# Kernel tuning notes

Hardware: AMD Instinct MI355X
Metric: run time of the kernel (lower is better)

## Reference

```python
import jax, jax.numpy as jnp
import numpy as np

B, M, P, L, L_EVAL = 16, 32, 16, 1024, 2048


def setup_inputs() -> dict:
    key = jax.random.key(0)
    ks = jax.random.split(key, 6)
    # sorted event times per (B, P) path via cumsum of positive steps
    steps = jax.random.uniform(ks[0], (B, P, L), minval=0.01, maxval=0.1)
    event_times = jnp.cumsum(steps, axis=-1)  # [B, P, L], strictly increasing
    norm_constants = jax.random.uniform(ks[1], (B,), minval=0.5, maxval=1.5)
    # queries on the ORIGINAL (unnormalised) time axis, spanning the event range
    t_max = event_times[..., -1]  # [B, P]
    q_norm = jax.random.uniform(ks[2], (B, P, L_EVAL)) * (1.05 * t_max)[..., None]
    query_times = q_norm * norm_constants[:, None, None]
    mu = jax.random.uniform(ks[3], (B, M, P, L), minval=0.05, maxval=1.0)
    alpha = jax.random.uniform(ks[4], (B, M, P, L), minval=0.05, maxval=2.0)
    beta = jax.random.uniform(ks[5], (B, M, P, L), minval=0.1, maxval=3.0)
    return {
        "query_times": query_times,
        "event_times": event_times,
        "mu": mu,
        "alpha": alpha,
        "beta": beta,
        "norm_constants": norm_constants,
    }


def _batched_searchsorted(a, v):
    # a: [B, P, L] sorted along last dim, v: [B, P, Q] -> int32 [B, P, Q]
    f = lambda av, vv: jnp.searchsorted(av, vv, side="left")
    return jax.vmap(jax.vmap(f))(a, v)


def reference(query_times, event_times, mu, alpha, beta, norm_constants):
    Bq, Pq, Le = query_times.shape
    Mm = mu.shape[1]
    # normalized_times=False path: map queries onto the normalised axis
    q_norm = query_times / norm_constants[:, None, None]  # [B, P, Le]
    # index of the latest event strictly before each query time
    last_idx = _batched_searchsorted(event_times, q_norm) - 1  # [B, P, Le]
    idx = jnp.clip(last_idx, 0, None)
    gidx = jnp.broadcast_to(idx[:, None, :, :], (Bq, Mm, Pq, Le))
    mu_last = jnp.take_along_axis(mu, gidx, axis=3)
    alpha_last = jnp.take_along_axis(alpha, gidx, axis=3)
    beta_last = jnp.take_along_axis(beta, gidx, axis=3)
    t_last = jnp.take_along_axis(event_times, idx, axis=2)  # [B, P, Le]
    t_last = jnp.where(last_idx == -1, jnp.zeros_like(t_last), t_last)
    delta_t = (q_norm - t_last)[:, None, :, :]  # [B, 1, P, Le]
    intensity = mu_last + (alpha_last - mu_last) * jnp.exp(-beta_last * delta_t)
    # map intensity back to the original scale
    intensity = intensity / norm_constants[:, None, None, None]
    return intensity
```

## Files before the change

kernel.cpp:

```cpp
#include <hip/hip_runtime.h>


constexpr int B  = 16;
constexpr int M  = 32;
constexpr int P  = 16;
constexpr int L  = 1024;
constexpr int LE = 2048;

__global__ __launch_bounds__(1024)
void hawkes_kernel(const float* __restrict__ qt,
                   const float* __restrict__ ev,
                   const float* __restrict__ mu,
                   const float* __restrict__ al,
                   const float* __restrict__ be,
                   const float* __restrict__ nc,
                   float* __restrict__ out)
{
    __shared__ float  s_ev[L];
    __shared__ float4 s_prm[2][L];

    const int bp = blockIdx.x;
    const int b  = bp >> 4;
    const int p  = bp & (P - 1);
    const int t  = threadIdx.x;

    const float norm     = nc[b];
    const float inv_norm = (float)(1.0 / (double)norm);

    const size_t row0 = ((size_t)b * M * P + p) * L;
    const size_t mstr = (size_t)P * L;

    const float e_in = ev[(size_t)bp * L + t];
    float rA_mu = mu[row0 + t],        rA_al = al[row0 + t],        rA_be = be[row0 + t];
    float rB_mu = mu[row0 + mstr + t], rB_al = al[row0 + mstr + t], rB_be = be[row0 + mstr + t];

    s_ev[t]     = e_in;
    s_prm[0][t] = make_float4(rA_mu, rA_al, rA_be, 0.0f);

    __syncthreads();

    const float2 q2 = *reinterpret_cast<const float2*>(qt + (size_t)bp * LE + 2 * t);
    int   idx0, idx1;
    float dt0, dt1;
    {
        float qn[2] = { __fmul_rn(q2.x, inv_norm), __fmul_rn(q2.y, inv_norm) };
        int lo[2] = {0, 0}, hi[2] = {L, L};
#pragma unroll
        for (int s = 0; s < 11; ++s) {
#pragma unroll
            for (int k = 0; k < 2; ++k) {
                if (lo[k] < hi[k]) {
                    const int mid = (lo[k] + hi[k]) >> 1;
                    if (s_ev[mid] < qn[k]) lo[k] = mid + 1; else hi[k] = mid;
                }
            }
        }
        const int l0 = lo[0] - 1, l1 = lo[1] - 1;
        idx0 = (l0 < 0) ? 0 : l0;   dt0 = qn[0] - ((l0 < 0) ? 0.0f : s_ev[idx0]);
        idx1 = (l1 < 0) ? 0 : l1;   dt1 = qn[1] - ((l1 < 0) ? 0.0f : s_ev[idx1]);
    }

    float* const obase = out + ((size_t)b * M * P + p) * LE + 2 * t;
    const size_t ostr  = (size_t)P * LE;

#define COMPUTE_ROW(BUF, mrow)                                                  \
    {                                                                           \
        const float4 v0 = s_prm[BUF][idx0];                                     \
        const float4 v1 = s_prm[BUF][idx1];                                     \
        float2 o;                                                               \
        o.x = fmaf(v0.y - v0.x, __expf(-v0.z * dt0), v0.x) * inv_norm;          \
        o.y = fmaf(v1.y - v1.x, __expf(-v1.z * dt1), v1.x) * inv_norm;          \
        *reinterpret_cast<float2*>(obase + (size_t)(mrow) * ostr) = o;          \
    }

#pragma unroll 1
    for (int m = 0; m < M; m += 2) {
        if (m + 2 < M) {
            const size_t r = row0 + (size_t)(m + 2) * mstr;
            rA_mu = mu[r + t];  rA_al = al[r + t];  rA_be = be[r + t];
        }
        COMPUTE_ROW(0, m)
        s_prm[1][t] = make_float4(rB_mu, rB_al, rB_be, 0.0f);
        __syncthreads();

        if (m + 3 < M) {
            const size_t r = row0 + (size_t)(m + 3) * mstr;
            rB_mu = mu[r + t];  rB_al = al[r + t];  rB_be = be[r + t];
        }
        COMPUTE_ROW(1, m + 1)
        if (m + 2 < M) {
            s_prm[0][t] = make_float4(rA_mu, rA_al, rA_be, 0.0f);
        }
        __syncthreads();
    }
#undef COMPUTE_ROW
}

extern "C" void kernel_launch(void* const* d_in, const int* in_sizes, int n_in,
                              void* d_out, int out_size, void* d_ws, size_t ws_size,
                              hipStream_t stream) {
    const float* qt = (const float*)d_in[0];
    const float* ev = (const float*)d_in[1];
    const float* mu = (const float*)d_in[2];
    const float* al = (const float*)d_in[3];
    const float* be = (const float*)d_in[4];
    const float* nc = (const float*)d_in[5];
    float* out = (float*)d_out;

    hawkes_kernel<<<B * P, 1024, 0, stream>>>(qt, ev, mu, al, be, nc, out);
}
```

Baseline: 33.83 us.

## Stage parameters as packed bf16 in shared memory, 16 rows per sync phase

Replaces the two-row double-buffered float4 staging with two phases of 16 rows each. All 16 rows' mu/alpha/beta are loaded up front into registers, packed as bf16 into uint2 shared slots, then gathered. This cuts the number of barriers and puts more loads in flight per thread. The bf16 packing halves shared-memory footprint and gather width but rounds the parameters to 8-bit mantissa, which risks exceeding the accuracy tolerance. It also greatly raises register pressure at 1024 threads per block.

New measurement: 35.11 us. 3.8% more time.

```diff
diff --git a/kernel.cpp b/kernel.cpp
--- a/kernel.cpp
+++ b/kernel.cpp
@@ -6,6 +6,12 @@
 constexpr int P  = 16;
 constexpr int L  = 1024;
 constexpr int LE = 2048;
+constexpr int RC = 16;
+
+__device__ __forceinline__ unsigned bf16rne(float x) {
+    const unsigned u = __float_as_uint(x);
+    return (u + 0x7FFFu + ((u >> 16) & 1u)) >> 16;
+}
 
 __global__ __launch_bounds__(1024)
 void hawkes_kernel(const float* __restrict__ qt,
@@ -16,8 +22,8 @@
                    const float* __restrict__ nc,
                    float* __restrict__ out)
 {
-    __shared__ float  s_ev[L];
-    __shared__ float4 s_prm[2][L];
+    __shared__ float s_ev[L];
+    __shared__ uint2 s_prm[RC][L];
 
     const int bp = blockIdx.x;
     const int b  = bp >> 4;
@@ -30,13 +36,13 @@
     const size_t row0 = ((size_t)b * M * P + p) * L;
     const size_t mstr = (size_t)P * L;
 
-    const float e_in = ev[(size_t)bp * L + t];
-    float rA_mu = mu[row0 + t],        rA_al = al[row0 + t],        rA_be = be[row0 + t];
-    float rB_mu = mu[row0 + mstr + t], rB_al = al[row0 + mstr + t], rB_be = be[row0 + mstr + t];
-
-    s_ev[t]     = e_in;
-    s_prm[0][t] = make_float4(rA_mu, rA_al, rA_be, 0.0f);
-
+    float vm[RC], va[RC], vb[RC];
+#pragma unroll
+    for (int r = 0; r < RC; ++r) {
+        const size_t a = row0 + (size_t)r * mstr + t;
+        vm[r] = mu[a];  va[r] = al[a];  vb[r] = be[a];
+    }
+    s_ev[t] = ev[(size_t)bp * L + t];
     __syncthreads();
 
     const float2 q2 = *reinterpret_cast<const float2*>(qt + (size_t)bp * LE + 2 * t);
@@ -60,40 +66,69 @@
         idx1 = (l1 < 0) ? 0 : l1;   dt1 = qn[1] - ((l1 < 0) ? 0.0f : s_ev[idx1]);
     }
 
+#pragma unroll
+    for (int r = 0; r < RC; ++r) {
+        s_prm[r][t] = make_uint2(bf16rne(vm[r]) | (bf16rne(va[r]) << 16),
+                                 bf16rne(vb[r]));
+    }
+    __syncthreads();
+
+#pragma unroll
+    for (int r = 0; r < RC; ++r) {
+        const size_t a = row0 + (size_t)(r + RC) * mstr + t;
+        vm[r] = mu[a];  va[r] = al[a];  vb[r] = be[a];
+    }
+
     float* const obase = out + ((size_t)b * M * P + p) * LE + 2 * t;
     const size_t ostr  = (size_t)P * LE;
 
-#define COMPUTE_ROW(BUF, mrow)                                                  \
-    {                                                                           \
-        const float4 v0 = s_prm[BUF][idx0];                                     \
-        const float4 v1 = s_prm[BUF][idx1];                                     \
-        float2 o;                                                               \
-        o.x = fmaf(v0.y - v0.x, __expf(-v0.z * dt0), v0.x) * inv_norm;          \
-        o.y = fmaf(v1.y - v1.x, __expf(-v1.z * dt1), v1.x) * inv_norm;          \
-        *reinterpret_cast<float2*>(obase + (size_t)(mrow) * ostr) = o;          \
+#pragma unroll
+    for (int r = 0; r < RC; ++r) {
+        const uint2 g0 = s_prm[r][idx0];
+        const uint2 g1 = s_prm[r][idx1];
+        float2 o;
+        {
+            const float m0 = __uint_as_float(g0.x << 16);
+            const float a0 = __uint_as_float(g0.x & 0xFFFF0000u);
+            const float b0 = __uint_as_float(g0.y << 16);
+            o.x = fmaf(a0 - m0, __expf(-b0 * dt0), m0) * inv_norm;
+        }
+        {
+            const float m1 = __uint_as_float(g1.x << 16);
+            const float a1 = __uint_as_float(g1.x & 0xFFFF0000u);
+            const float b1 = __uint_as_float(g1.y << 16);
+            o.y = fmaf(a1 - m1, __expf(-b1 * dt1), m1) * inv_norm;
+        }
+        *reinterpret_cast<float2*>(obase + (size_t)r * ostr) = o;
     }
+    __syncthreads();
 
-#pragma unroll 1
-    for (int m = 0; m < M; m += 2) {
-        if (m + 2 < M) {
-            const size_t r = row0 + (size_t)(m + 2) * mstr;
-            rA_mu = mu[r + t];  rA_al = al[r + t];  rA_be = be[r + t];
+#pragma unroll
+    for (int r = 0; r < RC; ++r) {
+        s_prm[r][t] = make_uint2(bf16rne(vm[r]) | (bf16rne(va[r]) << 16),
+                                 bf16rne(vb[r]));
+    }
+    __syncthreads();
+
+#pragma unroll
+    for (int r = 0; r < RC; ++r) {
+        const uint2 g0 = s_prm[r][idx0];
+        const uint2 g1 = s_prm[r][idx1];
+        float2 o;
+        {
+            const float m0 = __uint_as_float(g0.x << 16);
+            const float a0 = __uint_as_float(g0.x & 0xFFFF0000u);
+            const float b0 = __uint_as_float(g0.y << 16);
+            o.x = fmaf(a0 - m0, __expf(-b0 * dt0), m0) * inv_norm;
         }
-        COMPUTE_ROW(0, m)
-        s_prm[1][t] = make_float4(rB_mu, rB_al, rB_be, 0.0f);
-        __syncthreads();
-
-        if (m + 3 < M) {
-            const size_t r = row0 + (size_t)(m + 3) * mstr;
-            rB_mu = mu[r + t];  rB_al = al[r + t];  rB_be = be[r + t];
+        {
+            const float m1 = __uint_as_float(g1.x << 16);
+            const float a1 = __uint_as_float(g1.x & 0xFFFF0000u);
+            const float b1 = __uint_as_float(g1.y << 16);
+            o.y = fmaf(a1 - m1, __expf(-b1 * dt1), m1) * inv_norm;
         }
-        COMPUTE_ROW(1, m + 1)
-        if (m + 2 < M) {
-            s_prm[0][t] = make_float4(rA_mu, rA_al, rA_be, 0.0f);
-        }
-        __syncthreads();
+        *reinterpret_cast<float2*>(obase + (size_t)(r + RC) * ostr) = o;
     }
-#undef COMPUTE_ROW
 }
 
 extern "C" void kernel_launch(void* const* d_in, const int* in_sizes, int n_in,
```

## Split queries across four workgroups, pack params as bf16, remap blocks per XCD

Applied to the files above, without the earlier changes.

Each (b,p) row is now handled by four 512-thread workgroups, each covering a quarter of the queries. That gives 1024 workgroups instead of 256, and block IDs are remapped so consecutive chunks land on the same XCD. The mu/alpha/beta parameters are converted to bf16 and packed into 8 bytes in shared memory, which shrinks LDS use and gather width. The cost is that each workgroup redundantly reloads the full parameter rows, roughly quadrupling global parameter reads. bf16 rounding of the parameters also loses precision and may break the accuracy tolerance.

Result: slower. 38.09 us (+12.6%).

```diff
diff --git a/kernel.cpp b/kernel.cpp
--- a/kernel.cpp
+++ b/kernel.cpp
@@ -6,8 +6,18 @@
 constexpr int P  = 16;
 constexpr int L  = 1024;
 constexpr int LE = 2048;
+constexpr int QC = 4;
+constexpr int T  = 512;
+constexpr int NWG  = B * P * QC;
+constexpr int NXCD = 8;
+constexpr int CPX  = NWG / NXCD;
 
-__global__ __launch_bounds__(1024)
+__device__ __forceinline__ unsigned bf16rne(float x) {
+    const unsigned u = __float_as_uint(x);
+    return (u + 0x7FFFu + ((u >> 16) & 1u)) >> 16;
+}
+
+__global__ __launch_bounds__(T)
 void hawkes_kernel(const float* __restrict__ qt,
                    const float* __restrict__ ev,
                    const float* __restrict__ mu,
@@ -16,10 +26,14 @@
                    const float* __restrict__ nc,
                    float* __restrict__ out)
 {
-    __shared__ float  s_ev[L];
-    __shared__ float4 s_prm[2][L];
+    __shared__ float s_ev[L];
+    __shared__ uint2 s_prm[2][L];
 
-    const int bp = blockIdx.x;
+    const int orig = blockIdx.x;
+    const int bid  = (orig % NXCD) * CPX + orig / NXCD;
+
+    const int bp = bid >> 2;
+    const int qc = bid & (QC - 1);
     const int b  = bp >> 4;
     const int p  = bp & (P - 1);
     const int t  = threadIdx.x;
@@ -30,66 +44,93 @@
     const size_t row0 = ((size_t)b * M * P + p) * L;
     const size_t mstr = (size_t)P * L;
 
-    const float e_in = ev[(size_t)bp * L + t];
-    float rA_mu = mu[row0 + t],        rA_al = al[row0 + t],        rA_be = be[row0 + t];
-    float rB_mu = mu[row0 + mstr + t], rB_al = al[row0 + mstr + t], rB_be = be[row0 + mstr + t];
-
-    s_ev[t]     = e_in;
-    s_prm[0][t] = make_float4(rA_mu, rA_al, rA_be, 0.0f);
-
+    {
+        const float2 e2 = *reinterpret_cast<const float2*>(ev + (size_t)bp * L + 2 * t);
+        s_ev[2 * t]     = e2.x;
+        s_ev[2 * t + 1] = e2.y;
+    }
+    float2 rAm, rAa, rAb, rBm, rBa, rBb;
+    {
+        const float* pm = mu + row0 + 2 * t;
+        const float* pa = al + row0 + 2 * t;
+        const float* pb = be + row0 + 2 * t;
+        rAm = *reinterpret_cast<const float2*>(pm);
+        rAa = *reinterpret_cast<const float2*>(pa);
+        rAb = *reinterpret_cast<const float2*>(pb);
+        rBm = *reinterpret_cast<const float2*>(pm + mstr);
+        rBa = *reinterpret_cast<const float2*>(pa + mstr);
+        rBb = *reinterpret_cast<const float2*>(pb + mstr);
+    }
+    {
+        uint4 w;
+        w.x = bf16rne(rAm.x) | (bf16rne(rAa.x) << 16);
+        w.y = bf16rne(rAb.x);
+        w.z = bf16rne(rAm.y) | (bf16rne(rAa.y) << 16);
+        w.w = bf16rne(rAb.y);
+        reinterpret_cast<uint4*>(s_prm[0])[t] = w;
+    }
     __syncthreads();
 
-    const float2 q2 = *reinterpret_cast<const float2*>(qt + (size_t)bp * LE + 2 * t);
-    int   idx0, idx1;
-    float dt0, dt1;
-    {
-        float qn[2] = { __fmul_rn(q2.x, inv_norm), __fmul_rn(q2.y, inv_norm) };
-        int lo[2] = {0, 0}, hi[2] = {L, L};
+    const float q  = qt[(size_t)bp * LE + (size_t)qc * T + t];
+    const float qn = __fmul_rn(q, inv_norm);
+    int lo = 0, hi = L;
 #pragma unroll
-        for (int s = 0; s < 11; ++s) {
-#pragma unroll
-            for (int k = 0; k < 2; ++k) {
-                if (lo[k] < hi[k]) {
-                    const int mid = (lo[k] + hi[k]) >> 1;
-                    if (s_ev[mid] < qn[k]) lo[k] = mid + 1; else hi[k] = mid;
-                }
-            }
+    for (int s = 0; s < 11; ++s) {
+        if (lo < hi) {
+            const int mid = (lo + hi) >> 1;
+            if (s_ev[mid] < qn) lo = mid + 1; else hi = mid;
         }
-        const int l0 = lo[0] - 1, l1 = lo[1] - 1;
-        idx0 = (l0 < 0) ? 0 : l0;   dt0 = qn[0] - ((l0 < 0) ? 0.0f : s_ev[idx0]);
-        idx1 = (l1 < 0) ? 0 : l1;   dt1 = qn[1] - ((l1 < 0) ? 0.0f : s_ev[idx1]);
     }
+    const int   last = lo - 1;
+    const int   idx  = (last < 0) ? 0    : last;
+    const float dt   = qn - ((last < 0) ? 0.0f : s_ev[idx]);
 
-    float* const obase = out + ((size_t)b * M * P + p) * LE + 2 * t;
+    float* const obase = out + ((size_t)b * M * P + p) * LE + (size_t)qc * T + t;
     const size_t ostr  = (size_t)P * LE;
 
-#define COMPUTE_ROW(BUF, mrow)                                                  \
-    {                                                                           \
-        const float4 v0 = s_prm[BUF][idx0];                                     \
-        const float4 v1 = s_prm[BUF][idx1];                                     \
-        float2 o;                                                               \
-        o.x = fmaf(v0.y - v0.x, __expf(-v0.z * dt0), v0.x) * inv_norm;          \
-        o.y = fmaf(v1.y - v1.x, __expf(-v1.z * dt1), v1.x) * inv_norm;          \
-        *reinterpret_cast<float2*>(obase + (size_t)(mrow) * ostr) = o;          \
+#define COMPUTE_ROW(BUF, mrow)                                                 \
+    {                                                                          \
+        const uint2 g  = s_prm[BUF][idx];                                      \
+        const float mm = __uint_as_float(g.x << 16);                           \
+        const float aa = __uint_as_float(g.x & 0xFFFF0000u);                   \
+        const float bb = __uint_as_float(g.y << 16);                           \
+        obase[(size_t)(mrow) * ostr] =                                         \
+            fmaf(aa - mm, __expf(-bb * dt), mm) * inv_norm;                    \
     }
 
 #pragma unroll 1
     for (int m = 0; m < M; m += 2) {
         if (m + 2 < M) {
-            const size_t r = row0 + (size_t)(m + 2) * mstr;
-            rA_mu = mu[r + t];  rA_al = al[r + t];  rA_be = be[r + t];
+            const size_t r = row0 + (size_t)(m + 2) * mstr + 2 * t;
+            rAm = *reinterpret_cast<const float2*>(mu + r);
+            rAa = *reinterpret_cast<const float2*>(al + r);
+            rAb = *reinterpret_cast<const float2*>(be + r);
         }
         COMPUTE_ROW(0, m)
-        s_prm[1][t] = make_float4(rB_mu, rB_al, rB_be, 0.0f);
+        {
+            uint4 w;
+            w.x = bf16rne(rBm.x) | (bf16rne(rBa.x) << 16);
+            w.y = bf16rne(rBb.x);
+            w.z = bf16rne(rBm.y) | (bf16rne(rBa.y) << 16);
+            w.w = bf16rne(rBb.y);
+            reinterpret_cast<uint4*>(s_prm[1])[t] = w;
+        }
         __syncthreads();
 
         if (m + 3 < M) {
-            const size_t r = row0 + (size_t)(m + 3) * mstr;
-            rB_mu = mu[r + t];  rB_al = al[r + t];  rB_be = be[r + t];
+            const size_t r = row0 + (size_t)(m + 3) * mstr + 2 * t;
+            rBm = *reinterpret_cast<const float2*>(mu + r);
+            rBa = *reinterpret_cast<const float2*>(al + r);
+            rBb = *reinterpret_cast<const float2*>(be + r);
         }
         COMPUTE_ROW(1, m + 1)
         if (m + 2 < M) {
-            s_prm[0][t] = make_float4(rA_mu, rA_al, rA_be, 0.0f);
+            uint4 w;
+            w.x = bf16rne(rAm.x) | (bf16rne(rAa.x) << 16);
+            w.y = bf16rne(rAb.x);
+            w.z = bf16rne(rAm.y) | (bf16rne(rAa.y) << 16);
+            w.w = bf16rne(rAb.y);
+            reinterpret_cast<uint4*>(s_prm[0])[t] = w;
         }
         __syncthreads();
     }
@@ -107,5 +148,5 @@
     const float* nc = (const float*)d_in[5];
     float* out = (float*)d_out;
 
-    hawkes_kernel<<<B * P, 1024, 0, stream>>>(qt, ev, mu, al, be, nc, out);
+    hawkes_kernel<<<NWG, T, 0, stream>>>(qt, ev, mu, al, be, nc, out);
 }
```

## Split queries across two workgroups per path with XCD-aware block remapping

Applied to the files above, without the earlier changes.

Launches two workgroups per (b,p) path, each handling half of the queries with one query per thread, which doubles the grid size. Block IDs are remapped so that the two halves of a path land on the same XCD and can share its L2 cache. Parameters move from packed float4 LDS arrays to separate per-field arrays, and outputs use nontemporal stores. The cost is that each path's parameter rows are loaded twice from global memory and the binary search is repeated.

Result: no change. 33.38 us (-1.3%).

```diff
diff --git a/kernel.cpp b/kernel.cpp
--- a/kernel.cpp
+++ b/kernel.cpp
@@ -6,6 +6,9 @@
 constexpr int P  = 16;
 constexpr int L  = 1024;
 constexpr int LE = 2048;
+constexpr int NWG  = B * P * 2;
+constexpr int NXCD = 8;
+constexpr int CPX  = NWG / NXCD;
 
 __global__ __launch_bounds__(1024)
 void hawkes_kernel(const float* __restrict__ qt,
@@ -16,13 +19,18 @@
                    const float* __restrict__ nc,
                    float* __restrict__ out)
 {
-    __shared__ float  s_ev[L];
-    __shared__ float4 s_prm[2][L];
+    __shared__ float s_ev[L];
+    __shared__ float s_mu[2][L];
+    __shared__ float s_al[2][L];
+    __shared__ float s_be[2][L];
 
-    const int bp = blockIdx.x;
-    const int b  = bp >> 4;
-    const int p  = bp & (P - 1);
-    const int t  = threadIdx.x;
+    const int hw  = blockIdx.x;
+    const int lid = (hw / NXCD) + (hw % NXCD) * CPX;
+    const int bp  = lid >> 1;
+    const int qh  = lid & 1;
+    const int b   = bp >> 4;
+    const int p   = bp & (P - 1);
+    const int t   = threadIdx.x;
 
     const float norm     = nc[b];
     const float inv_norm = (float)(1.0 / (double)norm);
@@ -34,44 +42,27 @@
     float rA_mu = mu[row0 + t],        rA_al = al[row0 + t],        rA_be = be[row0 + t];
     float rB_mu = mu[row0 + mstr + t], rB_al = al[row0 + mstr + t], rB_be = be[row0 + mstr + t];
 
-    s_ev[t]     = e_in;
-    s_prm[0][t] = make_float4(rA_mu, rA_al, rA_be, 0.0f);
+    s_ev[t]    = e_in;
+    s_mu[0][t] = rA_mu;  s_al[0][t] = rA_al;  s_be[0][t] = rA_be;
 
     __syncthreads();
 
-    const float2 q2 = *reinterpret_cast<const float2*>(qt + (size_t)bp * LE + 2 * t);
-    int   idx0, idx1;
-    float dt0, dt1;
-    {
-        float qn[2] = { __fmul_rn(q2.x, inv_norm), __fmul_rn(q2.y, inv_norm) };
-        int lo[2] = {0, 0}, hi[2] = {L, L};
+    const float q  = qt[(size_t)bp * LE + (size_t)qh * 1024 + t];
+    const float qn = __fmul_rn(q, inv_norm);
+    int lo = 0, hi = L;
 #pragma unroll
-        for (int s = 0; s < 11; ++s) {
-#pragma unroll
-            for (int k = 0; k < 2; ++k) {
-                if (lo[k] < hi[k]) {
-                    const int mid = (lo[k] + hi[k]) >> 1;
-                    if (s_ev[mid] < qn[k]) lo[k] = mid + 1; else hi[k] = mid;
-                }
-            }
+    for (int s = 0; s < 11; ++s) {
+        if (lo < hi) {
+            const int mid = (lo + hi) >> 1;
+            if (s_ev[mid] < qn) lo = mid + 1; else hi = mid;
         }
-        const int l0 = lo[0] - 1, l1 = lo[1] - 1;
-        idx0 = (l0 < 0) ? 0 : l0;   dt0 = qn[0] - ((l0 < 0) ? 0.0f : s_ev[idx0]);
-        idx1 = (l1 < 0) ? 0 : l1;   dt1 = qn[1] - ((l1 < 0) ? 0.0f : s_ev[idx1]);
     }
+    const int   last = lo - 1;
+    const int   idx  = (last < 0) ? 0    : last;
+    const float dt   = qn - ((last < 0) ? 0.0f : s_ev[idx]);
 
-    float* const obase = out + ((size_t)b * M * P + p) * LE + 2 * t;
+    float* const obase = out + ((size_t)b * M * P + p) * LE + (size_t)qh * 1024 + t;
     const size_t ostr  = (size_t)P * LE;
-
-#define COMPUTE_ROW(BUF, mrow)                                                  \
-    {                                                                           \
-        const float4 v0 = s_prm[BUF][idx0];                                     \
-        const float4 v1 = s_prm[BUF][idx1];                                     \
-        float2 o;                                                               \
-        o.x = fmaf(v0.y - v0.x, __expf(-v0.z * dt0), v0.x) * inv_norm;          \
-        o.y = fmaf(v1.y - v1.x, __expf(-v1.z * dt1), v1.x) * inv_norm;          \
-        *reinterpret_cast<float2*>(obase + (size_t)(mrow) * ostr) = o;          \
-    }
 
 #pragma unroll 1
     for (int m = 0; m < M; m += 2) {
@@ -79,21 +70,30 @@
             const size_t r = row0 + (size_t)(m + 2) * mstr;
             rA_mu = mu[r + t];  rA_al = al[r + t];  rA_be = be[r + t];
         }
-        COMPUTE_ROW(0, m)
-        s_prm[1][t] = make_float4(rB_mu, rB_al, rB_be, 0.0f);
+        {
+            const float m0 = s_mu[0][idx], a0 = s_al[0][idx], b0 = s_be[0][idx];
+            __builtin_nontemporal_store(
+                fmaf(a0 - m0, __expf(-b0 * dt), m0) * inv_norm,
+                obase + (size_t)m * ostr);
+        }
+        s_mu[1][t] = rB_mu;  s_al[1][t] = rB_al;  s_be[1][t] = rB_be;
         __syncthreads();
 
         if (m + 3 < M) {
             const size_t r = row0 + (size_t)(m + 3) * mstr;
             rB_mu = mu[r + t];  rB_al = al[r + t];  rB_be = be[r + t];
         }
-        COMPUTE_ROW(1, m + 1)
+        {
+            const float m0 = s_mu[1][idx], a0 = s_al[1][idx], b0 = s_be[1][idx];
+            __builtin_nontemporal_store(
+                fmaf(a0 - m0, __expf(-b0 * dt), m0) * inv_norm,
+                obase + (size_t)(m + 1) * ostr);
+        }
         if (m + 2 < M) {
-            s_prm[0][t] = make_float4(rA_mu, rA_al, rA_be, 0.0f);
+            s_mu[0][t] = rA_mu;  s_al[0][t] = rA_al;  s_be[0][t] = rA_be;
         }
         __syncthreads();
     }
-#undef COMPUTE_ROW
 }
 
 extern "C" void kernel_launch(void* const* d_in, const int* in_sizes, int n_in,
@@ -107,5 +107,5 @@
     const float* nc = (const float*)d_in[5];
     float* out = (float*)d_out;
 
-    hawkes_kernel<<<B * P, 1024, 0, stream>>>(qt, ev, mu, al, be, nc, out);
+    hawkes_kernel<<<NWG, 1024, 0, stream>>>(qt, ev, mu, al, be, nc, out);
 }
```
